# Performance work log

Hardware: AMD Instinct MI355X
Metric: run time of the kernel (lower is better)

Reference implementation:

```python
import jax, jax.numpy as jnp
import numpy as np

B, A, F, S = 8192, 128, 16, 8

def setup_inputs() -> dict:
    key = jax.random.key(0)
    k1, k2, k3, k4 = jax.random.split(key, 4)
    c_iso = jax.random.normal(k1, (B, A, F), dtype=jnp.float32)
    int_iso = jax.random.uniform(k2, (B, A, F), dtype=jnp.float32)
    segment = jax.random.randint(k3, (B, A), 0, S, dtype=jnp.int64)
    charges = jax.random.normal(k4, (B, S), dtype=jnp.float32)
    return {"c_iso": c_iso, "int_iso": int_iso, "segment": segment, "charges": charges}

def reference(c_iso, int_iso, segment, charges):
    # c_iso, int_iso: [B, A, F]; segment: [B, A] in [0, S); charges: [B, S]
    b, a, f = c_iso.shape
    s = charges.shape[1]
    # global segment id per atom, flattened over batch (as in torch segment_r)
    seg_flat = (jnp.arange(b, dtype=segment.dtype)[:, None] * s + segment).reshape(-1)  # [B*A]
    c = c_iso.reshape(-1, f)   # [B*A, F]
    q = int_iso.reshape(-1, f)  # [B*A, F]
    nseg = b * s
    # KKT system [[2I, q],[-q^T, 0]] x = [2c; -charge] per segment has closed form
    # x = c - q * (q.c - charge) / (q.q)
    qc = jax.ops.segment_sum(jnp.sum(c * q, axis=-1), seg_flat, num_segments=nseg)  # [B*S]
    qq = jax.ops.segment_sum(jnp.sum(q * q, axis=-1), seg_flat, num_segments=nseg)  # [B*S]
    lam = (qc - charges.reshape(-1)) / qq  # [B*S] (half the Lagrange multiplier)
    x = c - q * lam[seg_flat][:, None]
    return x.reshape(b, a, f)
```

## Files before the change

kernel.cpp:

```cpp
#include <hip/hip_runtime.h>
#include <hip/hip_bf16.h>


#define B_ 8192
#define A_ 128
#define F_ 16
#define S_ 8

__global__ __launch_bounds__(A_) void qp_seg_norm_kernel(
    const float* __restrict__ c_iso,
    const float* __restrict__ int_iso,
    const int*   __restrict__ segment,
    const float* __restrict__ charges,
    float*       __restrict__ out)
{
    const int b = blockIdx.x;
    const int a = threadIdx.x;

    __shared__ float s_qc[S_];
    __shared__ float s_qq[S_];
    __shared__ float s_lam[S_];

    if (a < S_) { s_qc[a] = 0.0f; s_qq[a] = 0.0f; }
    __syncthreads();

    const size_t base = ((size_t)b * A_ + a) * F_;
    const float4* cp = reinterpret_cast<const float4*>(c_iso + base);
    const float4* qp = reinterpret_cast<const float4*>(int_iso + base);

    float4 cv[4], qv[4];
#pragma unroll
    for (int j = 0; j < 4; ++j) { cv[j] = cp[j]; qv[j] = qp[j]; }

    float cq = 0.0f, qq = 0.0f;
#pragma unroll
    for (int j = 0; j < 4; ++j) {
        cq += cv[j].x * qv[j].x + cv[j].y * qv[j].y
            + cv[j].z * qv[j].z + cv[j].w * qv[j].w;
        qq += qv[j].x * qv[j].x + qv[j].y * qv[j].y
            + qv[j].z * qv[j].z + qv[j].w * qv[j].w;
    }

    const int s = segment[(size_t)b * A_ + a];
    atomicAdd(&s_qc[s], cq);
    atomicAdd(&s_qq[s], qq);
    __syncthreads();

    if (a < S_) {
        const float charge = charges[(size_t)b * S_ + a];
        s_lam[a] = (s_qc[a] - charge) / s_qq[a];
    }
    __syncthreads();

    const float lam = s_lam[s];

    float4* op = reinterpret_cast<float4*>(out + base);
#pragma unroll
    for (int j = 0; j < 4; ++j) {
        float4 r;
        r.x = cv[j].x - qv[j].x * lam;
        r.y = cv[j].y - qv[j].y * lam;
        r.z = cv[j].z - qv[j].z * lam;
        r.w = cv[j].w - qv[j].w * lam;
        op[j] = r;
    }
}

extern "C" void kernel_launch(void* const* d_in, const int* in_sizes, int n_in,
                              void* d_out, int out_size, void* d_ws, size_t ws_size,
                              hipStream_t stream) {
    const float* c_iso   = (const float*)d_in[0];
    const float* int_iso = (const float*)d_in[1];
    const int*   segment = (const int*)d_in[2];
    const float* charges = (const float*)d_in[3];
    float* out = (float*)d_out;

    qp_seg_norm_kernel<<<B_, A_, 0, stream>>>(c_iso, int_iso, segment, charges, out);
}
```

Measured before the change: 38.11 us.

## Map one wavefront per batch with coalesced float4 access and no block barriers

Each 64-lane wavefront now handles a whole batch, reading c and q as contiguous float4 vectors strided by lane so each load instruction is fully coalesced. The per-atom segment id is read per vector, and partial sums go into per-wave shared arrays through shared-memory atomics. Four batches share a 256-thread block, and the block-wide __syncthreads are replaced by __threadfence_block, relying on wavefront lockstep execution. That reliance on implicit wave synchrony is fragile, and the shared-memory atomic count rises from 2 to 16 per lane.

Measured after the change: 63.42 us. 66.4% more time.

```diff
diff --git a/kernel.cpp b/kernel.cpp
--- a/kernel.cpp
+++ b/kernel.cpp
@@ -7,62 +7,72 @@
 #define F_ 16
 #define S_ 8
 
-__global__ __launch_bounds__(A_) void qp_seg_norm_kernel(
+#define WAVES_PER_BLOCK 4
+#define VEC_PER_BATCH (A_ * F_ / 4)
+#define VEC_PER_LANE  (VEC_PER_BATCH / 64)
+
+__global__ __launch_bounds__(64 * WAVES_PER_BLOCK) void qp_seg_norm_kernel(
     const float* __restrict__ c_iso,
     const float* __restrict__ int_iso,
     const int*   __restrict__ segment,
     const float* __restrict__ charges,
     float*       __restrict__ out)
 {
-    const int b = blockIdx.x;
-    const int a = threadIdx.x;
+    const int w    = threadIdx.x >> 6;
+    const int lane = threadIdx.x & 63;
+    const int b    = blockIdx.x * WAVES_PER_BLOCK + w;
 
-    __shared__ float s_qc[S_];
-    __shared__ float s_qq[S_];
-    __shared__ float s_lam[S_];
+    __shared__ float s_qc[WAVES_PER_BLOCK][S_];
+    __shared__ float s_qq[WAVES_PER_BLOCK][S_];
+    __shared__ float s_lam[WAVES_PER_BLOCK][S_];
 
-    if (a < S_) { s_qc[a] = 0.0f; s_qq[a] = 0.0f; }
-    __syncthreads();
+    if (lane < S_) { s_qc[w][lane] = 0.0f; s_qq[w][lane] = 0.0f; }
 
-    const size_t base = ((size_t)b * A_ + a) * F_;
-    const float4* cp = reinterpret_cast<const float4*>(c_iso + base);
-    const float4* qp = reinterpret_cast<const float4*>(int_iso + base);
+    const size_t vbase = (size_t)b * VEC_PER_BATCH;
+    const float4* cp = reinterpret_cast<const float4*>(c_iso)   + vbase;
+    const float4* qp = reinterpret_cast<const float4*>(int_iso) + vbase;
+    const int*    sp = segment + (size_t)b * A_;
 
-    float4 cv[4], qv[4];
+    float4 cv[VEC_PER_LANE], qv[VEC_PER_LANE];
+    int    sg[VEC_PER_LANE];
+
 #pragma unroll
-    for (int j = 0; j < 4; ++j) { cv[j] = cp[j]; qv[j] = qp[j]; }
-
-    float cq = 0.0f, qq = 0.0f;
-#pragma unroll
-    for (int j = 0; j < 4; ++j) {
-        cq += cv[j].x * qv[j].x + cv[j].y * qv[j].y
-            + cv[j].z * qv[j].z + cv[j].w * qv[j].w;
-        qq += qv[j].x * qv[j].x + qv[j].y * qv[j].y
-            + qv[j].z * qv[j].z + qv[j].w * qv[j].w;
+    for (int j = 0; j < VEC_PER_LANE; ++j) {
+        const int idx = j * 64 + lane;
+        cv[j] = cp[idx];
+        qv[j] = qp[idx];
+        sg[j] = sp[idx >> 2];
     }
 
-    const int s = segment[(size_t)b * A_ + a];
-    atomicAdd(&s_qc[s], cq);
-    atomicAdd(&s_qq[s], qq);
-    __syncthreads();
+#pragma unroll
+    for (int j = 0; j < VEC_PER_LANE; ++j) {
+        const float cq = cv[j].x * qv[j].x + cv[j].y * qv[j].y
+                       + cv[j].z * qv[j].z + cv[j].w * qv[j].w;
+        const float qq = qv[j].x * qv[j].x + qv[j].y * qv[j].y
+                       + qv[j].z * qv[j].z + qv[j].w * qv[j].w;
+        atomicAdd(&s_qc[w][sg[j]], cq);
+        atomicAdd(&s_qq[w][sg[j]], qq);
+    }
 
-    if (a < S_) {
-        const float charge = charges[(size_t)b * S_ + a];
-        s_lam[a] = (s_qc[a] - charge) / s_qq[a];
+    __threadfence_block();
+
+    if (lane < S_) {
+        const float charge = charges[(size_t)b * S_ + lane];
+        s_lam[w][lane] = (s_qc[w][lane] - charge) / s_qq[w][lane];
     }
-    __syncthreads();
+    __threadfence_block();
 
-    const float lam = s_lam[s];
-
-    float4* op = reinterpret_cast<float4*>(out + base);
+    float4* op = reinterpret_cast<float4*>(out) + vbase;
 #pragma unroll
-    for (int j = 0; j < 4; ++j) {
+    for (int j = 0; j < VEC_PER_LANE; ++j) {
+        const float lam = s_lam[w][sg[j]];
+        const int idx = j * 64 + lane;
         float4 r;
         r.x = cv[j].x - qv[j].x * lam;
         r.y = cv[j].y - qv[j].y * lam;
         r.z = cv[j].z - qv[j].z * lam;
         r.w = cv[j].w - qv[j].w * lam;
-        op[j] = r;
+        op[idx] = r;
     }
 }
 
@@ -75,5 +85,6 @@
     const float* charges = (const float*)d_in[3];
     float* out = (float*)d_out;
 
-    qp_seg_norm_kernel<<<B_, A_, 0, stream>>>(c_iso, int_iso, segment, charges, out);
+    qp_seg_norm_kernel<<<B_ / WAVES_PER_BLOCK, 64 * WAVES_PER_BLOCK, 0, stream>>>(
+        c_iso, int_iso, segment, charges, out);
 }
```
